# Performance work log

Hardware: AMD Instinct MI355X
Metric: run time of the kernel (lower is better)

Reference implementation:

```python
import jax, jax.numpy as jnp
import numpy as np

QMAX = 127.0

def fake_quant(t):
    # per-tensor symmetric int8 quantize -> dequantize (STE for grads)
    scale = jnp.maximum(jnp.max(jnp.abs(t)) / QMAX, 1e-8)
    q = jnp.clip(jnp.round(t / scale), -QMAX, QMAX) * scale
    return t + jax.lax.stop_gradient(q - t)

def qlinear(x, W, b):
    # quantized linear: int8 activations x int8 weights, dequantized output
    return fake_quant(x) @ fake_quant(W).T + b

def hardsigmoid(t):
    return jnp.clip(t / 6.0 + 0.5, 0.0, 1.0)

def setup_inputs() -> dict:
    key = jax.random.key(0)
    ks = jax.random.split(key, 5)
    B, C, H, W_, R = 64, 1024, 28, 28, 256
    return {
        "x":  jax.random.normal(ks[0], (B, C, H, W_), dtype=jnp.float32),
        "W1": jax.random.normal(ks[1], (R, C), dtype=jnp.float32) * (1.0 / np.sqrt(C)),
        "b1": jax.random.normal(ks[2], (R,), dtype=jnp.float32) * 0.01,
        "W2": jax.random.normal(ks[3], (C, R), dtype=jnp.float32) * (1.0 / np.sqrt(R)),
        "b2": jax.random.normal(ks[4], (C,), dtype=jnp.float32) * 0.01,
    }

def reference(x, W1, b1, W2, b2):
    b, c, h, w = x.shape
    # 1. quantize input
    xq = fake_quant(x)
    # 2. quantized global avgpool -> [b, c]
    se = fake_quant(jnp.mean(xq, axis=(2, 3)))
    # 3-4. quantized fc1 -> fp32 relu
    se = jax.nn.relu(qlinear(se, W1, b1))
    # 5. quantized fc2 -> fp32
    se = qlinear(se, W2, b2)
    # 6. hardsigmoid gate
    se = hardsigmoid(se)
    # 7. broadcast scale in fp32 (original input path was fp32)
    return x * se[:, :, None, None]
```

## Files before the change

kernel.cpp:

```cpp
#include <hip/hip_runtime.h>

#define QMAX 127.0f

#define B_  64
#define C_  1024
#define H_  28
#define W__ 28
#define HW_ 784
#define R_  256
#define N_TOTAL (B_*C_*HW_)
#define N4_TOTAL (N_TOTAL/4)

#define MEAN_OFF 8
#define H_OFF    (MEAN_OFF + B_*C_)
#define G_OFF    (H_OFF + B_*R_)

__global__ __launch_bounds__(64) void k_init(float* ws) {
    if (threadIdx.x < 8) ws[threadIdx.x] = 0.0f;
}

__global__ __launch_bounds__(256) void k_absmax4(const float4* __restrict__ p, int n4,
                                                 float* __restrict__ out) {
    float m = 0.0f;
    for (int i = blockIdx.x * blockDim.x + threadIdx.x; i < n4; i += gridDim.x * blockDim.x) {
        float4 v = p[i];
        m = fmaxf(m, fmaxf(fmaxf(fabsf(v.x), fabsf(v.y)), fmaxf(fabsf(v.z), fabsf(v.w))));
    }
    for (int o = 32; o > 0; o >>= 1) m = fmaxf(m, __shfl_down(m, o, 64));
    __shared__ float sm[4];
    int wid = threadIdx.x >> 6, lane = threadIdx.x & 63;
    if (lane == 0) sm[wid] = m;
    __syncthreads();
    if (threadIdx.x == 0) {
        float bm = fmaxf(fmaxf(sm[0], sm[1]), fmaxf(sm[2], sm[3]));
        atomicMax((unsigned int*)out, __float_as_uint(bm));
    }
}

__global__ __launch_bounds__(256) void k_mean(const float* __restrict__ x,
                                              const float* __restrict__ ws,
                                              float* __restrict__ mean) {
    int wid = threadIdx.x >> 6, lane = threadIdx.x & 63;
    int bc = blockIdx.x * 4 + wid;
    float s = fmaxf(ws[0] / QMAX, 1e-8f);
    float rs = 1.0f / s;
    const float4* p = (const float4*)(x + (size_t)bc * HW_);
    int isum = 0;
    #pragma unroll
    for (int j = 0; j < 4; j++) {
        int idx = lane + 64 * j;
        if (idx < HW_ / 4) {
            float4 v = p[idx];
            isum += (int)fminf(fmaxf(rintf(v.x * rs), -QMAX), QMAX);
            isum += (int)fminf(fmaxf(rintf(v.y * rs), -QMAX), QMAX);
            isum += (int)fminf(fmaxf(rintf(v.z * rs), -QMAX), QMAX);
            isum += (int)fminf(fmaxf(rintf(v.w * rs), -QMAX), QMAX);
        }
    }
    for (int o = 32; o > 0; o >>= 1) isum += __shfl_down(isum, o, 64);
    if (lane == 0) mean[bc] = (float)isum * s / (float)HW_;
}

__global__ __launch_bounds__(256) void k_fc1(const float* __restrict__ ws,
                                             const float* __restrict__ W1,
                                             const float* __restrict__ b1,
                                             float* __restrict__ h) {
    int wid = threadIdx.x >> 6, lane = threadIdx.x & 63;
    int out = blockIdx.x * 4 + wid;
    int b = out >> 8, r = out & 255;
    float s2  = fmaxf(ws[3] / QMAX, 1e-8f);
    float s2p = fmaxf((QMAX * s2) / QMAX, 1e-8f);
    float sw  = fmaxf(ws[1] / QMAX, 1e-8f);
    const float* mrow = ws + MEAN_OFF + b * C_;
    const float* wrow = W1 + r * C_;
    int idot = 0;
    for (int c = lane; c < C_; c += 64) {
        int ka = (int)fminf(fmaxf(rintf(mrow[c] / s2), -QMAX), QMAX);
        int kw = (int)fminf(fmaxf(rintf(wrow[c] / sw), -QMAX), QMAX);
        idot += ka * kw;
    }
    for (int o = 32; o > 0; o >>= 1) idot += __shfl_down(idot, o, 64);
    if (lane == 0) {
        float v = (float)idot * (s2p * sw) + b1[r];
        h[out] = fmaxf(v, 0.0f);
    }
}

__global__ __launch_bounds__(256) void k_fc2(const float* __restrict__ ws,
                                             const float* __restrict__ W2,
                                             const float* __restrict__ b2,
                                             float* __restrict__ gate) {
    int wid = threadIdx.x >> 6, lane = threadIdx.x & 63;
    int out = blockIdx.x * 4 + wid;
    int b = out >> 10, c = out & 1023;
    float sh = fmaxf(ws[4] / QMAX, 1e-8f);
    float sw = fmaxf(ws[2] / QMAX, 1e-8f);
    const float* hrow = ws + H_OFF + b * R_;
    const float* wrow = W2 + c * R_;
    int idot = 0;
    #pragma unroll
    for (int r0 = 0; r0 < R_; r0 += 64) {
        int r = r0 + lane;
        int ka = (int)fminf(fmaxf(rintf(hrow[r] / sh), -QMAX), QMAX);
        int kw = (int)fminf(fmaxf(rintf(wrow[r] / sw), -QMAX), QMAX);
        idot += ka * kw;
    }
    for (int o = 32; o > 0; o >>= 1) idot += __shfl_down(idot, o, 64);
    if (lane == 0) {
        float t = (float)idot * (sh * sw) + b2[c];
        gate[out] = fminf(fmaxf(t / 6.0f + 0.5f, 0.0f), 1.0f);
    }
}

__global__ __launch_bounds__(256) void k_scale(const float* __restrict__ x,
                                               const float* __restrict__ gate,
                                               float* __restrict__ out) {
    const float4* xv = (const float4*)x;
    float4* ov = (float4*)out;
    for (unsigned i = blockIdx.x * blockDim.x + threadIdx.x; i < (unsigned)N4_TOTAL;
         i += gridDim.x * blockDim.x) {
        unsigned bc = i / (HW_ / 4);
        float g = gate[bc];
        float4 v = xv[i];
        v.x *= g; v.y *= g; v.z *= g; v.w *= g;
        ov[i] = v;
    }
}

extern "C" void kernel_launch(void* const* d_in, const int* in_sizes, int n_in,
                              void* d_out, int out_size, void* d_ws, size_t ws_size,
                              hipStream_t stream) {
    const float* x  = (const float*)d_in[0];
    const float* W1 = (const float*)d_in[1];
    const float* b1 = (const float*)d_in[2];
    const float* W2 = (const float*)d_in[3];
    const float* b2 = (const float*)d_in[4];
    float* out = (float*)d_out;
    float* ws  = (float*)d_ws;

    k_init<<<1, 64, 0, stream>>>(ws);
    k_absmax4<<<2048, 256, 0, stream>>>((const float4*)x,  N4_TOTAL,      ws + 0);
    k_absmax4<<<64,   256, 0, stream>>>((const float4*)W1, (R_*C_)/4,     ws + 1);
    k_absmax4<<<64,   256, 0, stream>>>((const float4*)W2, (C_*R_)/4,     ws + 2);
    k_mean<<<(B_*C_)/4, 256, 0, stream>>>(x, ws, ws + MEAN_OFF);
    k_absmax4<<<32, 256, 0, stream>>>((const float4*)(ws + MEAN_OFF), (B_*C_)/4, ws + 3);
    k_fc1<<<(B_*R_)/4, 256, 0, stream>>>(ws, W1, b1, ws + H_OFF);
    k_absmax4<<<16, 256, 0, stream>>>((const float4*)(ws + H_OFF), (B_*R_)/4, ws + 4);
    k_fc2<<<(B_*C_)/4, 256, 0, stream>>>(ws, W2, b2, ws + G_OFF);
    k_scale<<<8192, 256, 0, stream>>>(x, ws + G_OFF, out);
}
```

Before: 471.1 us.

## Fuse absmax reductions into neighbouring stages and drop atomics and init kernel

Replaces the ten-launch pipeline with five kernels. Per-block partial maxima are written to the workspace and reduced by the next stage instead of using atomicMax, which removes the init kernel and the separate absmax launches for mean and hidden. Mean, fc1 and fc2 now give each wave several rows, use float4 loads and multiply by reciprocals. The final scale kernel uses nontemporal stores. The price is that every block redundantly re-reduces 1024 partials, and the large x tensor is still read three times.

```diff
diff --git a/kernel.cpp b/kernel.cpp
--- a/kernel.cpp
+++ b/kernel.cpp
@@ -1,129 +1,199 @@
 #include <hip/hip_runtime.h>
 
 #define QMAX 127.0f
-
-#define B_  64
-#define C_  1024
-#define H_  28
-#define W__ 28
-#define HW_ 784
-#define R_  256
-#define N_TOTAL (B_*C_*HW_)
-#define N4_TOTAL (N_TOTAL/4)
-
-#define MEAN_OFF 8
-#define H_OFF    (MEAN_OFF + B_*C_)
-#define G_OFF    (H_OFF + B_*R_)
-
-__global__ __launch_bounds__(64) void k_init(float* ws) {
-    if (threadIdx.x < 8) ws[threadIdx.x] = 0.0f;
-}
-
-__global__ __launch_bounds__(256) void k_absmax4(const float4* __restrict__ p, int n4,
-                                                 float* __restrict__ out) {
-    float m = 0.0f;
-    for (int i = blockIdx.x * blockDim.x + threadIdx.x; i < n4; i += gridDim.x * blockDim.x) {
-        float4 v = p[i];
-        m = fmaxf(m, fmaxf(fmaxf(fabsf(v.x), fabsf(v.y)), fmaxf(fabsf(v.z), fabsf(v.w))));
-    }
-    for (int o = 32; o > 0; o >>= 1) m = fmaxf(m, __shfl_down(m, o, 64));
-    __shared__ float sm[4];
-    int wid = threadIdx.x >> 6, lane = threadIdx.x & 63;
-    if (lane == 0) sm[wid] = m;
+#define B_   64
+#define C_   1024
+#define HW_  784
+#define R_   256
+#define NROW 65536
+#define N4_TOTAL 12845056
+#define ROW4 196
+
+typedef float fx4 __attribute__((ext_vector_type(4)));
+
+#define PX_OFF   0
+#define PW1_OFF  1024
+#define PW2_OFF  2048
+#define PM_OFF   3072
+#define PH_OFF   4096
+#define MEAN_OFF 8192
+#define H_OFF    (MEAN_OFF + NROW)
+#define GATE_OFF (H_OFF + B_*R_)
+
+__device__ __forceinline__ float block_max(float v, volatile float* sm) {
+    #pragma unroll
+    for (int o = 32; o > 0; o >>= 1) v = fmaxf(v, __shfl_xor(v, o, 64));
+    int lane = threadIdx.x & 63, wid = threadIdx.x >> 6;
+    if (lane == 0) sm[wid] = v;
     __syncthreads();
+    float r = fmaxf(fmaxf(sm[0], sm[1]), fmaxf(sm[2], sm[3]));
+    __syncthreads();
+    return r;
+}
+
+__device__ __forceinline__ float amax4(float4 v) {
+    return fmaxf(fmaxf(fabsf(v.x), fabsf(v.y)), fmaxf(fabsf(v.z), fabsf(v.w)));
+}
+
+__device__ __forceinline__ int q1(float v, float rs) {
+    return (int)fminf(fmaxf(rintf(v * rs), -QMAX), QMAX);
+}
+
+__device__ __forceinline__ int q4sum(float4 v, float rs) {
+    return q1(v.x, rs) + q1(v.y, rs) + q1(v.z, rs) + q1(v.w, rs);
+}
+
+__global__ __launch_bounds__(256) void kA(const float4* __restrict__ x,
+                                          const float4* __restrict__ w1,
+                                          const float4* __restrict__ w2,
+                                          float* __restrict__ ws) {
+    __shared__ float sm[4];
+    int tid = blockIdx.x * 256 + threadIdx.x;
+    float mx = 0.0f;
+    #pragma unroll 7
+    for (int j = 0; j < 49; j++) mx = fmaxf(mx, amax4(x[tid + j * 262144]));
+    float m1 = (tid < 65536) ? amax4(w1[tid]) : 0.0f;
+    float m2 = (tid < 65536) ? amax4(w2[tid]) : 0.0f;
+    float bx  = block_max(mx, sm);
+    float b1m = block_max(m1, sm);
+    float b2m = block_max(m2, sm);
     if (threadIdx.x == 0) {
-        float bm = fmaxf(fmaxf(sm[0], sm[1]), fmaxf(sm[2], sm[3]));
-        atomicMax((unsigned int*)out, __float_as_uint(bm));
-    }
-}
-
-__global__ __launch_bounds__(256) void k_mean(const float* __restrict__ x,
-                                              const float* __restrict__ ws,
-                                              float* __restrict__ mean) {
-    int wid = threadIdx.x >> 6, lane = threadIdx.x & 63;
-    int bc = blockIdx.x * 4 + wid;
-    float s = fmaxf(ws[0] / QMAX, 1e-8f);
+        ws[PX_OFF  + blockIdx.x] = bx;
+        ws[PW1_OFF + blockIdx.x] = b1m;
+        ws[PW2_OFF + blockIdx.x] = b2m;
+    }
+}
+
+__global__ __launch_bounds__(256) void kB(const float* __restrict__ x,
+                                          float* __restrict__ ws) {
+    __shared__ float sm[4];
+    int t = threadIdx.x;
+    const float* px = ws + PX_OFF;
+    float v = fmaxf(fmaxf(px[t], px[t + 256]), fmaxf(px[t + 512], px[t + 768]));
+    float gmax = block_max(v, sm);
+    float s  = fmaxf(gmax / QMAX, 1e-8f);
     float rs = 1.0f / s;
-    const float4* p = (const float4*)(x + (size_t)bc * HW_);
-    int isum = 0;
-    #pragma unroll
-    for (int j = 0; j < 4; j++) {
-        int idx = lane + 64 * j;
-        if (idx < HW_ / 4) {
-            float4 v = p[idx];
-            isum += (int)fminf(fmaxf(rintf(v.x * rs), -QMAX), QMAX);
-            isum += (int)fminf(fmaxf(rintf(v.y * rs), -QMAX), QMAX);
-            isum += (int)fminf(fmaxf(rintf(v.z * rs), -QMAX), QMAX);
-            isum += (int)fminf(fmaxf(rintf(v.w * rs), -QMAX), QMAX);
-        }
-    }
-    for (int o = 32; o > 0; o >>= 1) isum += __shfl_down(isum, o, 64);
-    if (lane == 0) mean[bc] = (float)isum * s / (float)HW_;
-}
-
-__global__ __launch_bounds__(256) void k_fc1(const float* __restrict__ ws,
-                                             const float* __restrict__ W1,
-                                             const float* __restrict__ b1,
-                                             float* __restrict__ h) {
-    int wid = threadIdx.x >> 6, lane = threadIdx.x & 63;
-    int out = blockIdx.x * 4 + wid;
-    int b = out >> 8, r = out & 255;
-    float s2  = fmaxf(ws[3] / QMAX, 1e-8f);
-    float s2p = fmaxf((QMAX * s2) / QMAX, 1e-8f);
-    float sw  = fmaxf(ws[1] / QMAX, 1e-8f);
-    const float* mrow = ws + MEAN_OFF + b * C_;
-    const float* wrow = W1 + r * C_;
-    int idot = 0;
-    for (int c = lane; c < C_; c += 64) {
-        int ka = (int)fminf(fmaxf(rintf(mrow[c] / s2), -QMAX), QMAX);
-        int kw = (int)fminf(fmaxf(rintf(wrow[c] / sw), -QMAX), QMAX);
-        idot += ka * kw;
-    }
-    for (int o = 32; o > 0; o >>= 1) idot += __shfl_down(idot, o, 64);
-    if (lane == 0) {
-        float v = (float)idot * (s2p * sw) + b1[r];
-        h[out] = fmaxf(v, 0.0f);
-    }
-}
-
-__global__ __launch_bounds__(256) void k_fc2(const float* __restrict__ ws,
-                                             const float* __restrict__ W2,
-                                             const float* __restrict__ b2,
-                                             float* __restrict__ gate) {
-    int wid = threadIdx.x >> 6, lane = threadIdx.x & 63;
-    int out = blockIdx.x * 4 + wid;
-    int b = out >> 10, c = out & 1023;
-    float sh = fmaxf(ws[4] / QMAX, 1e-8f);
-    float sw = fmaxf(ws[2] / QMAX, 1e-8f);
-    const float* hrow = ws + H_OFF + b * R_;
-    const float* wrow = W2 + c * R_;
-    int idot = 0;
-    #pragma unroll
-    for (int r0 = 0; r0 < R_; r0 += 64) {
-        int r = r0 + lane;
-        int ka = (int)fminf(fmaxf(rintf(hrow[r] / sh), -QMAX), QMAX);
-        int kw = (int)fminf(fmaxf(rintf(wrow[r] / sw), -QMAX), QMAX);
-        idot += ka * kw;
-    }
-    for (int o = 32; o > 0; o >>= 1) idot += __shfl_down(idot, o, 64);
-    if (lane == 0) {
-        float t = (float)idot * (sh * sw) + b2[c];
-        gate[out] = fminf(fmaxf(t / 6.0f + 0.5f, 0.0f), 1.0f);
-    }
-}
-
-__global__ __launch_bounds__(256) void k_scale(const float* __restrict__ x,
-                                               const float* __restrict__ gate,
-                                               float* __restrict__ out) {
-    const float4* xv = (const float4*)x;
-    float4* ov = (float4*)out;
-    for (unsigned i = blockIdx.x * blockDim.x + threadIdx.x; i < (unsigned)N4_TOTAL;
-         i += gridDim.x * blockDim.x) {
-        unsigned bc = i / (HW_ / 4);
-        float g = gate[bc];
-        float4 v = xv[i];
-        v.x *= g; v.y *= g; v.z *= g; v.w *= g;
-        ov[i] = v;
+    int wid = t >> 6, lane = t & 63;
+    int gw = blockIdx.x * 4 + wid;
+    float wmax = 0.0f;
+    #pragma unroll
+    for (int k = 0; k < 8; k++) {
+        int bc = gw * 8 + k;
+        const float4* p = (const float4*)(x + (size_t)bc * HW_);
+        int isum = 0;
+        #pragma unroll
+        for (int j = 0; j < 3; j++) isum += q4sum(p[lane + 64 * j], rs);
+        if (lane < 4) isum += q4sum(p[192 + lane], rs);
+        #pragma unroll
+        for (int o = 32; o > 0; o >>= 1) isum += __shfl_xor(isum, o, 64);
+        float m = (float)isum * s / 784.0f;
+        if (lane == 0) ws[MEAN_OFF + bc] = m;
+        wmax = fmaxf(wmax, fabsf(m));
+    }
+    float bm = block_max(wmax, sm);
+    if (t == 0) ws[PM_OFF + blockIdx.x] = bm;
+}
+
+__global__ __launch_bounds__(256) void kC(const float* __restrict__ W1,
+                                          const float* __restrict__ b1,
+                                          float* __restrict__ ws) {
+    __shared__ float sm[4];
+    int t = threadIdx.x;
+    const float* pm = ws + PM_OFF;
+    const float* pw = ws + PW1_OFF;
+    float vm = fmaxf(fmaxf(pm[t], pm[t + 256]), fmaxf(pm[t + 512], pm[t + 768]));
+    float vw = fmaxf(fmaxf(pw[t], pw[t + 256]), fmaxf(pw[t + 512], pw[t + 768]));
+    float mmax = block_max(vm, sm);
+    float wmx  = block_max(vw, sm);
+    float s2  = fmaxf(mmax / QMAX, 1e-8f);
+    float s2q = fmaxf((QMAX * s2) / QMAX, 1e-8f);
+    float sw  = fmaxf(wmx / QMAX, 1e-8f);
+    float rs2 = 1.0f / s2, rsw = 1.0f / sw;
+    int wid = t >> 6, lane = t & 63;
+    int gw = blockIdx.x * 4 + wid;
+    float hmax = 0.0f;
+    #pragma unroll
+    for (int k = 0; k < 4; k++) {
+        int out = gw * 4 + k;
+        int b = out >> 8, r = out & 255;
+        const float4* mrow = (const float4*)(ws + MEAN_OFF + b * C_);
+        const float4* wrow = (const float4*)(W1 + r * C_);
+        int idot = 0;
+        #pragma unroll
+        for (int j = 0; j < 4; j++) {
+            float4 mv = mrow[lane + 64 * j];
+            float4 wv = wrow[lane + 64 * j];
+            idot += q1(mv.x, rs2) * q1(wv.x, rsw) + q1(mv.y, rs2) * q1(wv.y, rsw)
+                  + q1(mv.z, rs2) * q1(wv.z, rsw) + q1(mv.w, rs2) * q1(wv.w, rsw);
+        }
+        #pragma unroll
+        for (int o = 32; o > 0; o >>= 1) idot += __shfl_xor(idot, o, 64);
+        float hv = fmaxf((float)idot * (s2q * sw) + b1[r], 0.0f);
+        if (lane == 0) ws[H_OFF + out] = hv;
+        hmax = fmaxf(hmax, hv);
+    }
+    float bh = block_max(hmax, sm);
+    if (t == 0) ws[PH_OFF + blockIdx.x] = bh;
+}
+
+__global__ __launch_bounds__(256) void kD(const float* __restrict__ W2,
+                                          const float* __restrict__ b2,
+                                          float* __restrict__ ws) {
+    __shared__ float sm[4];
+    int t = threadIdx.x;
+    const float* ph = ws + PH_OFF;
+    const float* pw = ws + PW2_OFF;
+    float vh = fmaxf(fmaxf(ph[t], ph[t + 256]), fmaxf(ph[t + 512], ph[t + 768]));
+    float vw = fmaxf(fmaxf(pw[t], pw[t + 256]), fmaxf(pw[t + 512], pw[t + 768]));
+    float hmx = block_max(vh, sm);
+    float wmx = block_max(vw, sm);
+    float sh = fmaxf(hmx / QMAX, 1e-8f);
+    float sw = fmaxf(wmx / QMAX, 1e-8f);
+    float rsh = 1.0f / sh, rsw = 1.0f / sw;
+    int wid = t >> 6, lane = t & 63;
+    int gw = blockIdx.x * 4 + wid;
+    #pragma unroll
+    for (int k = 0; k < 16; k++) {
+        int out = gw * 16 + k;
+        int b = out >> 10, c = out & 1023;
+        const float4* hrow = (const float4*)(ws + H_OFF + b * R_);
+        const float4* wrow = (const float4*)(W2 + c * R_);
+        float4 hv = hrow[lane];
+        float4 wv = wrow[lane];
+        int idot = q1(hv.x, rsh) * q1(wv.x, rsw) + q1(hv.y, rsh) * q1(wv.y, rsw)
+                 + q1(hv.z, rsh) * q1(wv.z, rsw) + q1(hv.w, rsh) * q1(wv.w, rsw);
+        #pragma unroll
+        for (int o = 32; o > 0; o >>= 1) idot += __shfl_xor(idot, o, 64);
+        if (lane == 0) {
+            float tv = (float)idot * (sh * sw) + b2[c];
+            ws[GATE_OFF + out] = fminf(fmaxf(tv / 6.0f + 0.5f, 0.0f), 1.0f);
+        }
+    }
+}
+
+__global__ __launch_bounds__(256) void kE(const float* __restrict__ x,
+                                          const float* __restrict__ ws,
+                                          float* __restrict__ out) {
+    int t = threadIdx.x;
+    int wid = t >> 6, lane = t & 63;
+    int gw = blockIdx.x * 4 + wid;
+    #pragma unroll
+    for (int k = 0; k < 8; k++) {
+        int bc = gw * 8 + k;
+        float g = ws[GATE_OFF + bc];
+        const fx4* p = (const fx4*)(x + (size_t)bc * HW_);
+        fx4* o = (fx4*)(out + (size_t)bc * HW_);
+        #pragma unroll
+        for (int j = 0; j < 3; j++) {
+            fx4 v = p[lane + 64 * j];
+            v *= g;
+            __builtin_nontemporal_store(v, &o[lane + 64 * j]);
+        }
+        if (lane < 4) {
+            fx4 v = p[192 + lane];
+            v *= g;
+            __builtin_nontemporal_store(v, &o[192 + lane]);
+        }
     }
 }
 
@@ -138,14 +208,9 @@
     float* out = (float*)d_out;
     float* ws  = (float*)d_ws;
 
-    k_init<<<1, 64, 0, stream>>>(ws);
-    k_absmax4<<<2048, 256, 0, stream>>>((const float4*)x,  N4_TOTAL,      ws + 0);
-    k_absmax4<<<64,   256, 0, stream>>>((const float4*)W1, (R_*C_)/4,     ws + 1);
-    k_absmax4<<<64,   256, 0, stream>>>((const float4*)W2, (C_*R_)/4,     ws + 2);
-    k_mean<<<(B_*C_)/4, 256, 0, stream>>>(x, ws, ws + MEAN_OFF);
-    k_absmax4<<<32, 256, 0, stream>>>((const float4*)(ws + MEAN_OFF), (B_*C_)/4, ws + 3);
-    k_fc1<<<(B_*R_)/4, 256, 0, stream>>>(ws, W1, b1, ws + H_OFF);
-    k_absmax4<<<16, 256, 0, stream>>>((const float4*)(ws + H_OFF), (B_*R_)/4, ws + 4);
-    k_fc2<<<(B_*C_)/4, 256, 0, stream>>>(ws, W2, b2, ws + G_OFF);
-    k_scale<<<8192, 256, 0, stream>>>(x, ws + G_OFF, out);
-}
+    kA<<<1024, 256, 0, stream>>>((const float4*)x, (const float4*)W1, (const float4*)W2, ws);
+    kB<<<2048, 256, 0, stream>>>(x, ws);
+    kC<<<1024, 256, 0, stream>>>(W1, b1, ws);
+    kD<<<1024, 256, 0, stream>>>(W2, b2, ws);
+    kE<<<2048, 256, 0, stream>>>(x, ws, out);
+}
```

Result: faster. 431.1 us (-8.5%).
